# Kernel optimization log

Measured on AMD Instinct MI355X. Metric: run time of the kernel, lower is better.

## Reference

```python
import jax, jax.numpy as jnp
import numpy as np

N_STACK = 32
ZERO_OFFSET = 1e-6
EPS = 1e-8
POW_EPS = 1e-12  # guard for 0**sharpen gradient


def _cos_sim(a, b):
    # a: [D] param, b: [B, D]; matches torch.cosine_similarity with eps=1e-8
    an = jnp.maximum(jnp.sqrt(jnp.sum(a * a)), EPS)
    bn = jnp.maximum(jnp.sqrt(jnp.sum(b * b, axis=-1)), EPS)
    return (b @ a) / (an * bn)


def _elu(x):
    return jnp.where(x > 0, x, jnp.expm1(x))


def setup_inputs() -> dict:
    key = jax.random.key(0)
    k0, k1, k2, k3 = jax.random.split(key, 4)
    B, T, D = 128, 256, 256
    return {
        "x": jax.random.normal(k0, (B, T, D), jnp.float32),
        "should_pop": jax.random.normal(k1, (D,), jnp.float32),
        "sharpen_pointer": jnp.array([5.0], jnp.float32),
        "latch_enable": jax.random.normal(k2, (D,), jnp.float32) * 0.01,
        "latch_init": jax.random.normal(k3, (B, D), jnp.float32),
    }


def _forward(x, should_pop, sharpen_pointer, latch_enable, latch_init):
    B, T, D = x.shape
    dtype = x.dtype
    stack0 = jnp.full((B, N_STACK, D), ZERO_OFFSET, dtype)
    ptr0 = jnp.full((B, N_STACK), ZERO_OFFSET, dtype).at[:, 0].set(1.0)
    sharpen = sharpen_pointer[0]

    def step(carry, inp):
        stack, ptr, latch = carry  # [B,N,D], [B,N], [B,D]
        # pop gate from PREVIOUS latch state (relay of length 1)
        pop = _elu(_cos_sim(should_pop, latch))            # [B]
        push = 1.0 - pop
        # push branch: advance pointer, write value at new slot
        p_push = jnp.roll(ptr, 1, axis=1)
        st_push = stack * (1.0 - p_push)[..., None] + inp[:, None, :] * p_push[..., None]
        # pop branch: erase current slot to zero_offset, retreat pointer
        st_pop = stack * (1.0 - ptr)[..., None] + ZERO_OFFSET * ptr[..., None]
        p_pop = jnp.roll(ptr, -1, axis=1)
        # superpose push/pop (null_op weight is exactly 0 in this module)
        new_stack = push[:, None, None] * st_push + pop[:, None, None] * st_pop
        new_ptr = push[:, None] * p_push + pop[:, None] * p_pop
        # sharpen pointer: relu, pow, renormalize
        p = jnp.maximum(jax.nn.relu(new_ptr), POW_EPS) ** sharpen
        p = p / jnp.maximum(jnp.sum(p, axis=1, keepdims=True), EPS)
        # read and gate output
        s = jnp.einsum('bnv,bn->bv', new_stack, p)
        out = pop[:, None] * s
        # latch update: gate = elu(cos(enable_param, inp)); dropout is eval-mode no-op
        g = _elu(_cos_sim(latch_enable, inp))
        new_latch = g[:, None] * inp + (1.0 - g)[:, None] * latch
        return (new_stack, p, new_latch), out

    _, outs = jax.lax.scan(step, (stack0, ptr0, latch_init), jnp.swapaxes(x, 0, 1))
    return jnp.swapaxes(outs, 0, 1)  # [B, T, D]


def reference(x, should_pop, sharpen_pointer, latch_enable, latch_init):
    return _forward(x, should_pop, sharpen_pointer, latch_enable, latch_init)
```

## Files before the change

### kernel.cpp

```cpp
#include <hip/hip_runtime.h>
#include <math.h>


#define NSTK 32
#define DDIM 256
#define ZO 1e-6f
#define EPSC 1e-8f
#define PEPS 1e-12f
#define TTILE 32

__device__ __forceinline__ float elu_f(float c) {
    return (c > 0.f) ? c : expm1f(c);
}

__global__ void gate4_kernel(const float* __restrict__ vecs,
                             const float* __restrict__ par,
                             float* __restrict__ gout,
                             int T) {
    const int b = blockIdx.y;
    const int t = blockIdx.x * 4 + (threadIdx.x >> 6);
    const int lane = threadIdx.x & 63;
    const float4 v = *(const float4*)(vecs + ((size_t)b * T + t) * DDIM + lane * 4);
    const float4 p = *(const float4*)(par + lane * 4);
    float r0 = v.x * p.x + v.y * p.y + v.z * p.z + v.w * p.w;
    float r1 = v.x * v.x + v.y * v.y + v.z * v.z + v.w * v.w;
    float r2 = p.x * p.x + p.y * p.y + p.z * p.z + p.w * p.w;
#pragma unroll
    for (int off = 32; off >= 1; off >>= 1) {
        r0 += __shfl_xor(r0, off, 64);
        r1 += __shfl_xor(r1, off, 64);
        r2 += __shfl_xor(r2, off, 64);
    }
    if (lane == 0) {
        const float c = r0 / (fmaxf(sqrtf(r2), EPSC) * fmaxf(sqrtf(r1), EPSC));
        gout[(size_t)b * T + t] = elu_f(c);
    }
}

__global__ void latch_scan_kernel(const float* __restrict__ x,
                                  const float* __restrict__ latch0,
                                  const float* __restrict__ g,
                                  float* __restrict__ L,
                                  int T) {
    const int b = blockIdx.x >> 2;
    const int dt = blockIdx.x & 3;
    const int d = dt * 64 + threadIdx.x;
    const float* xb = x + (size_t)b * T * DDIM + d;
    const float* gb = g + (size_t)b * T;
    float* Lb = L + (size_t)b * T * DDIM + d;
    float l = latch0[(size_t)b * DDIM + d];
    for (int c = 0; c < T; c += 32) {
        float xv[32], gv[32];
#pragma unroll
        for (int i = 0; i < 32; i++) xv[i] = xb[(size_t)(c + i) * DDIM];
#pragma unroll
        for (int i = 0; i < 32; i++) gv[i] = gb[c + i];
#pragma unroll
        for (int i = 0; i < 32; i++) {
            Lb[(size_t)(c + i) * DDIM] = l;
            l = fmaf(gv[i], xv[i] - l, l);
        }
    }
}

__global__ void ptr_scan_kernel(const float* __restrict__ pop_arr,
                                const float* __restrict__ sharpen_ptr,
                                float* __restrict__ scal,
                                int T) {
    const int b = blockIdx.x;
    const int n = threadIdx.x & 31;
    const bool act = threadIdx.x < 32;
    const float sharpen = sharpen_ptr[0];
    const bool sharp5 = (sharpen == 5.0f);
    const float* popb = pop_arr + (size_t)b * T;
    float* scb = scal + (size_t)b * T * 128;

    float p = (n == 0) ? 1.0f : ZO;
    for (int t = 0; t < T; t++) {
        const float pop = popb[t];
        const float push = 1.0f - pop;
        const float pp = __shfl(p, (n + 31) & 31, 32);
        const float pn = __shfl(p, (n + 1) & 31, 32);
        float np = fmaf(push, pp, pop * pn);
        float q = fmaxf(np, PEPS);
        float q5;
        if (sharp5) { const float q2 = q * q; q5 = q2 * q2 * q; }
        else        { q5 = exp2f(sharpen * log2f(q)); }
        float s = q5;
        s += __shfl_xor(s, 16, 32);
        s += __shfl_xor(s, 8, 32);
        s += __shfl_xor(s, 4, 32);
        s += __shfl_xor(s, 2, 32);
        s += __shfl_xor(s, 1, 32);
        const float inv = 1.0f / fmaxf(s, EPSC);
        const float pnew = q5 * inv;
        if (act) {
            float* row = scb + (size_t)t * 128;
            row[n]      = fmaf(push, -pp, push) + fmaf(pop, -p, pop);
            row[32 + n] = push * pp;
            row[64 + n] = pop * p * ZO;
            row[96 + n] = pop * pnew;
        }
        p = pnew;
    }
}

__launch_bounds__(256, 2)
__global__ void stack_kernel(const float* __restrict__ x,
                             const float* __restrict__ scal,
                             float* __restrict__ out,
                             int T) {
    const int b = blockIdx.y;
    const int dtile = blockIdx.x;
    const int tid = threadIdx.x;
    const int wave = tid >> 6;
    const int lane = tid & 63;
    const int dsub = lane & 15;
    const int ng = lane >> 4;

    __shared__ float sc_s[2][TTILE * 128];
    __shared__ float x_s[2][TTILE * 64];

    const float* scb = scal + (size_t)b * T * 128;
    const float* xtb = x + (size_t)b * T * DDIM + dtile * 64;
    float* ob = out + (size_t)b * T * DDIM + dtile * 64 + wave * 16 + dsub;

    const int f0 = tid, f1 = tid + 256;
    const int tr0 = f0 >> 4, dq0 = (f0 & 15) * 4;
    const int tr1 = f1 >> 4, dq1 = (f1 & 15) * 4;

    float4 sreg[4], xreg[2];

    auto load_tile = [&](int t0) {
        const float4* sg = (const float4*)(scb + (size_t)t0 * 128);
        sreg[0] = sg[tid];
        sreg[1] = sg[tid + 256];
        sreg[2] = sg[tid + 512];
        sreg[3] = sg[tid + 768];
        xreg[0] = *(const float4*)(xtb + (size_t)(t0 + tr0) * DDIM + dq0);
        xreg[1] = *(const float4*)(xtb + (size_t)(t0 + tr1) * DDIM + dq1);
    };
    auto store_tile = [&](int buf) {
        float4* ss = (float4*)sc_s[buf];
        ss[tid] = sreg[0];
        ss[tid + 256] = sreg[1];
        ss[tid + 512] = sreg[2];
        ss[tid + 768] = sreg[3];
        float4* xs = (float4*)x_s[buf];
        xs[f0] = xreg[0];
        xs[f1] = xreg[1];
    };

    float st[8];
#pragma unroll
    for (int j = 0; j < 8; j++) st[j] = ZO;

    load_tile(0);
    store_tile(0);
    __syncthreads();

    const int NT = T / TTILE;
    for (int tile = 0; tile < NT; tile++) {
        if (tile + 1 < NT) load_tile((tile + 1) * TTILE);
        const float* scl = sc_s[tile & 1];
        const float* xl = x_s[tile & 1] + wave * 16 + dsub;
        const int tglob = tile * TTILE;
#pragma unroll 4
        for (int tl = 0; tl < TTILE; tl++) {
            const float4* sc4 = (const float4*)(scl + tl * 128) + ng * 2;
            const float4 a0 = sc4[0],  a1 = sc4[1];
            const float4 b0 = sc4[8],  b1 = sc4[9];
            const float4 g0 = sc4[16], g1 = sc4[17];
            const float4 w0 = sc4[24], w1 = sc4[25];
            const float xv = xl[tl * 64];

            float acc;
            st[0] = fmaf(a0.x, st[0], fmaf(b0.x, xv, g0.x)); acc  = st[0] * w0.x;
            st[1] = fmaf(a0.y, st[1], fmaf(b0.y, xv, g0.y)); acc += st[1] * w0.y;
            st[2] = fmaf(a0.z, st[2], fmaf(b0.z, xv, g0.z)); acc += st[2] * w0.z;
            st[3] = fmaf(a0.w, st[3], fmaf(b0.w, xv, g0.w)); acc += st[3] * w0.w;
            st[4] = fmaf(a1.x, st[4], fmaf(b1.x, xv, g1.x)); acc += st[4] * w1.x;
            st[5] = fmaf(a1.y, st[5], fmaf(b1.y, xv, g1.y)); acc += st[5] * w1.y;
            st[6] = fmaf(a1.z, st[6], fmaf(b1.z, xv, g1.z)); acc += st[6] * w1.z;
            st[7] = fmaf(a1.w, st[7], fmaf(b1.w, xv, g1.w)); acc += st[7] * w1.w;

            acc += __shfl_xor(acc, 16, 64);
            acc += __shfl_xor(acc, 32, 64);
            if (ng == 0) ob[(size_t)(tglob + tl) * DDIM] = acc;
        }
        if (tile + 1 < NT) store_tile((tile + 1) & 1);
        __syncthreads();
    }
}

__launch_bounds__(256, 1)
__global__ void neuralstack_kernel(const float* __restrict__ x,
                                   const float* __restrict__ should_pop,
                                   const float* __restrict__ sharpen_ptr,
                                   const float* __restrict__ latch_enable,
                                   const float* __restrict__ latch_init,
                                   float* __restrict__ out,
                                   int T) {
    const int b = blockIdx.x;
    const int tid = threadIdx.x;
    const int wave = tid >> 6;
    const int lane = tid & 63;
    __shared__ float red[2][16];
    const float sp_d = should_pop[tid];
    const float le_d = latch_enable[tid];
    const float sharpen = sharpen_ptr[0];
    float latch = latch_init[(size_t)b * DDIM + tid];
    float a0 = sp_d * sp_d, a1 = le_d * le_d;
#pragma unroll
    for (int off = 32; off >= 1; off >>= 1) {
        a0 += __shfl_xor(a0, off, 64);
        a1 += __shfl_xor(a1, off, 64);
    }
    if (lane == 0) { red[0][wave * 4] = a0; red[0][wave * 4 + 1] = a1; }
    __syncthreads();
    const float an_sp = fmaxf(sqrtf(red[0][0] + red[0][4] + red[0][8] + red[0][12]), EPSC);
    const float an_le = fmaxf(sqrtf(red[0][1] + red[0][5] + red[0][9] + red[0][13]), EPSC);
    __syncthreads();
    float st[NSTK], ptr[NSTK];
#pragma unroll
    for (int n = 0; n < NSTK; n++) { st[n] = ZO; ptr[n] = (n == 0) ? 1.0f : ZO; }
    const float* xb = x + (size_t)b * T * DDIM + tid;
    float* ob = out + (size_t)b * T * DDIM + tid;
    const bool sharp5 = (sharpen == 5.0f);
    float inp = xb[0];
    for (int t = 0; t < T; t++) {
        const int tn = (t + 1 < T) ? (t + 1) : (T - 1);
        const float inp_next = xb[(size_t)tn * DDIM];
        float r0 = sp_d * latch, r1 = latch * latch, r2 = le_d * inp, r3 = inp * inp;
#pragma unroll
        for (int off = 32; off >= 1; off >>= 1) {
            r0 += __shfl_xor(r0, off, 64);
            r1 += __shfl_xor(r1, off, 64);
            r2 += __shfl_xor(r2, off, 64);
            r3 += __shfl_xor(r3, off, 64);
        }
        const int buf = t & 1;
        if (lane == 0) {
            red[buf][wave * 4] = r0; red[buf][wave * 4 + 1] = r1;
            red[buf][wave * 4 + 2] = r2; red[buf][wave * 4 + 3] = r3;
        }
        __syncthreads();
        const float s0 = red[buf][0] + red[buf][4] + red[buf][8] + red[buf][12];
        const float s1 = red[buf][1] + red[buf][5] + red[buf][9] + red[buf][13];
        const float s2 = red[buf][2] + red[buf][6] + red[buf][10] + red[buf][14];
        const float s3 = red[buf][3] + red[buf][7] + red[buf][11] + red[buf][15];
        const float pop = elu_f(s0 / (an_sp * fmaxf(sqrtf(s1), EPSC)));
        const float push = 1.0f - pop;
        const float g = elu_f(s2 / (an_le * fmaxf(sqrtf(s3), EPSC)));
        float q[NSTK];
#pragma unroll
        for (int n = 0; n < NSTK; n++) {
            const float pp = ptr[(n + NSTK - 1) & (NSTK - 1)];
            const float pn = ptr[(n + 1) & (NSTK - 1)];
            q[n] = fmaxf(push * pp + pop * pn, PEPS);
        }
        if (sharp5) {
#pragma unroll
            for (int n = 0; n < NSTK; n++) { const float v = q[n], v2 = v * v; q[n] = v2 * v2 * v; }
        } else {
#pragma unroll
            for (int n = 0; n < NSTK; n++) q[n] = exp2f(sharpen * log2f(q[n]));
        }
        float qa = 0.f, qb = 0.f, qc = 0.f, qd = 0.f;
#pragma unroll
        for (int n = 0; n < NSTK; n += 4) { qa += q[n]; qb += q[n+1]; qc += q[n+2]; qd += q[n+3]; }
        const float inv = 1.0f / fmaxf((qa + qb) + (qc + qd), EPSC);
        float sacc = 0.f;
#pragma unroll
        for (int n = 0; n < NSTK; n++) {
            const float pp = ptr[(n + NSTK - 1) & (NSTK - 1)];
            const float pc = ptr[n];
            const float ns = push * (st[n] + pp * (inp - st[n])) + pop * (st[n] + pc * (ZO - st[n]));
            st[n] = ns;
            sacc += ns * (q[n] * inv);
        }
#pragma unroll
        for (int n = 0; n < NSTK; n++) ptr[n] = q[n] * inv;
        ob[(size_t)t * DDIM] = pop * sacc;
        latch = fmaf(g, inp - latch, latch);
        inp = inp_next;
    }
}

extern "C" void kernel_launch(void* const* d_in, const int* in_sizes, int n_in,
                              void* d_out, int out_size, void* d_ws, size_t ws_size,
                              hipStream_t stream) {
    const float* x = (const float*)d_in[0];
    const float* should_pop = (const float*)d_in[1];
    const float* sharpen_ptr = (const float*)d_in[2];
    const float* latch_enable = (const float*)d_in[3];
    const float* latch_init = (const float*)d_in[4];
    float* out = (float*)d_out;

    const int D = in_sizes[1];
    const int B = in_sizes[4] / D;
    const int T = in_sizes[0] / in_sizes[4];
    (void)n_in; (void)out_size;

    const size_t BT = (size_t)B * T;
    const size_t off_g = 0;
    const size_t off_pop = BT;
    const size_t off_L = 2 * BT;
    const size_t off_scal = off_L + BT * D;
    const size_t need_floats = off_scal + BT * 128;

    if (ws_size < need_floats * sizeof(float) || D != DDIM ||
        (T % TTILE) != 0 || (T % 4) != 0) {
        neuralstack_kernel<<<B, 256, 0, stream>>>(x, should_pop, sharpen_ptr,
                                                  latch_enable, latch_init, out, T);
        return;
    }

    float* ws = (float*)d_ws;
    float* g = ws + off_g;
    float* pop = ws + off_pop;
    float* L = ws + off_L;
    float* scal = ws + off_scal;

    gate4_kernel<<<dim3(T / 4, B), 256, 0, stream>>>(x, latch_enable, g, T);
    latch_scan_kernel<<<B * 4, 64, 0, stream>>>(x, latch_init, g, L, T);
    gate4_kernel<<<dim3(T / 4, B), 256, 0, stream>>>(L, should_pop, pop, T);
    ptr_scan_kernel<<<B, 64, 0, stream>>>(pop, sharpen_ptr, scal, T);
    stack_kernel<<<dim3(D / 64, B), 256, 0, stream>>>(x, scal, out, T);
}
```

Measured before the change: 260.9 us.

## Pack two batches per wave in pointer scan, use DPP reductions and deferred normalization

The pointer scan kernel now handles two batch rows per 64-lane wave, one per half-wave, where previously half of each wave sat idle. Pop values are staged in shared memory first. The serial loop carries an unnormalized pointer plus its inverse norm, so the divide no longer sits on the shuffle dependency chain. The 32-lane sum uses DPP and ds_swizzle in place of generic shuffles. Together these aim to shorten the per-step serial latency and halve the block count. In exchange the kernel needs an even batch size and T of at most 1024, and rounding shifts slightly from the rescaled recurrence.

```diff
diff --git a/kernel.cpp b/kernel.cpp
--- a/kernel.cpp
+++ b/kernel.cpp
@@ -8,9 +8,26 @@
 #define EPSC 1e-8f
 #define PEPS 1e-12f
 #define TTILE 32
+#define MAXT 1024
 
 __device__ __forceinline__ float elu_f(float c) {
     return (c > 0.f) ? c : expm1f(c);
+}
+
+__device__ __forceinline__ float dpp_xor1(float x) {
+    return __int_as_float(__builtin_amdgcn_update_dpp(0, __float_as_int(x), 0xB1, 0xF, 0xF, true));
+}
+__device__ __forceinline__ float dpp_xor2(float x) {
+    return __int_as_float(__builtin_amdgcn_update_dpp(0, __float_as_int(x), 0x4E, 0xF, 0xF, true));
+}
+__device__ __forceinline__ float dpp_halfmirror(float x) {
+    return __int_as_float(__builtin_amdgcn_update_dpp(0, __float_as_int(x), 0x141, 0xF, 0xF, true));
+}
+__device__ __forceinline__ float dpp_mirror(float x) {
+    return __int_as_float(__builtin_amdgcn_update_dpp(0, __float_as_int(x), 0x140, 0xF, 0xF, true));
+}
+__device__ __forceinline__ float swz_xor16(float x) {
+    return __int_as_float(__builtin_amdgcn_ds_swizzle(__float_as_int(x), 0x401F));
 }
 
 __global__ void gate4_kernel(const float* __restrict__ vecs,
@@ -63,45 +80,56 @@
     }
 }
 
+__launch_bounds__(64, 1)
 __global__ void ptr_scan_kernel(const float* __restrict__ pop_arr,
                                 const float* __restrict__ sharpen_ptr,
                                 float* __restrict__ scal,
                                 int T) {
-    const int b = blockIdx.x;
-    const int n = threadIdx.x & 31;
-    const bool act = threadIdx.x < 32;
+    const int b0 = blockIdx.x * 2;
+    const int tid = threadIdx.x;
+    const int n = tid & 31;
+    const int grp = tid >> 5;
     const float sharpen = sharpen_ptr[0];
     const bool sharp5 = (sharpen == 5.0f);
-    const float* popb = pop_arr + (size_t)b * T;
-    float* scb = scal + (size_t)b * T * 128;
-
-    float p = (n == 0) ? 1.0f : ZO;
+
+    __shared__ float pops[2 * MAXT];
+    for (int i = tid; i < 2 * T; i += 64) pops[i] = pop_arr[(size_t)b0 * T + i];
+    __syncthreads();
+    const float* popg = pops + grp * T;
+
+    float* scb = scal + (size_t)(b0 + grp) * T * 128;
+
+    float u = (n == 0) ? 1.0f : ZO;
+    float invu = 1.0f;
+
+#pragma unroll 2
     for (int t = 0; t < T; t++) {
-        const float pop = popb[t];
+        const float pop = popg[t];
         const float push = 1.0f - pop;
-        const float pp = __shfl(p, (n + 31) & 31, 32);
-        const float pn = __shfl(p, (n + 1) & 31, 32);
-        float np = fmaf(push, pp, pop * pn);
-        float q = fmaxf(np, PEPS);
-        float q5;
-        if (sharp5) { const float q2 = q * q; q5 = q2 * q2 * q; }
-        else        { q5 = exp2f(sharpen * log2f(q)); }
-        float s = q5;
-        s += __shfl_xor(s, 16, 32);
-        s += __shfl_xor(s, 8, 32);
-        s += __shfl_xor(s, 4, 32);
-        s += __shfl_xor(s, 2, 32);
-        s += __shfl_xor(s, 1, 32);
-        const float inv = 1.0f / fmaxf(s, EPSC);
-        const float pnew = q5 * inv;
-        if (act) {
-            float* row = scb + (size_t)t * 128;
-            row[n]      = fmaf(push, -pp, push) + fmaf(pop, -p, pop);
-            row[32 + n] = push * pp;
-            row[64 + n] = pop * p * ZO;
-            row[96 + n] = pop * pnew;
-        }
-        p = pnew;
+        const float up = __shfl(u, (n + 31) & 31, 32);
+        const float un = __shfl(u, (n + 1) & 31, 32);
+        const float r = fmaf(push, up, pop * un);
+        const float np = r * invu;
+        const float q = fmaxf(np, PEPS);
+        float unew;
+        if (sharp5) { const float q2 = q * q, q4 = q2 * q2; unew = q4 * q; }
+        else        { unew = exp2f(sharpen * log2f(q)); }
+        float s = unew;
+        s += dpp_xor1(s);
+        s += dpp_xor2(s);
+        s += dpp_halfmirror(s);
+        s += dpp_mirror(s);
+        s += swz_xor16(s);
+        const float invn = 1.0f / fmaxf(s, EPSC);
+        const float p = u * invu;
+        const float ppn = up * invu;
+        const float pnew = unew * invn;
+        float* row = scb + (size_t)t * 128;
+        row[n]      = fmaf(push, -ppn, push) + fmaf(pop, -p, pop);
+        row[32 + n] = push * ppn;
+        row[64 + n] = pop * p * ZO;
+        row[96 + n] = pop * pnew;
+        u = unew; invu = invn;
     }
 }
 
@@ -310,7 +338,7 @@
     const size_t need_floats = off_scal + BT * 128;
 
     if (ws_size < need_floats * sizeof(float) || D != DDIM ||
-        (T % TTILE) != 0 || (T % 4) != 0) {
+        (T % TTILE) != 0 || (T % 4) != 0 || (B % 2) != 0 || T > MAXT) {
         neuralstack_kernel<<<B, 256, 0, stream>>>(x, should_pop, sharpen_ptr,
                                                   latch_enable, latch_init, out, T);
         return;
@@ -325,6 +353,6 @@
     gate4_kernel<<<dim3(T / 4, B), 256, 0, stream>>>(x, latch_enable, g, T);
     latch_scan_kernel<<<B * 4, 64, 0, stream>>>(x, latch_init, g, L, T);
     gate4_kernel<<<dim3(T / 4, B), 256, 0, stream>>>(L, should_pop, pop, T);
-    ptr_scan_kernel<<<B, 64, 0, stream>>>(pop, sharpen_ptr, scal, T);
+    ptr_scan_kernel<<<B / 2, 64, 0, stream>>>(pop, sharpen_ptr, scal, T);
     stack_kernel<<<dim3(D / 64, B), 256, 0, stream>>>(x, scal, out, T);
 }
```

After: 227.3 us. 1.15x faster.
